# Kernel tuning notes

Hardware: AMD Instinct MI355X
Metric: run time of the kernel (lower is better)

The kernel has to match this reference:

```python
import jax, jax.numpy as jnp
import numpy as np
import math

B, L, E, H, G = 2, 128, 1024, 16, 8
D = E // H   # head_dim = 64
R = H // G   # query heads per kv head = 2


def setup_inputs() -> dict:
    key = jax.random.key(0)
    ks = jax.random.split(key, 12)
    def nrm(k, shape, s=1.0):
        return jax.random.normal(k, shape, dtype=jnp.float32) * s
    return {
        "Q": nrm(ks[0], (B, L, E)),
        "K": nrm(ks[1], (B, L, E)),
        "V": nrm(ks[2], (B, L, E)),
        "rpe": nrm(ks[3], (B, L, L, E)),
        "ln_g": jnp.ones((E,), jnp.float32),
        "ln_b": jnp.zeros((E,), jnp.float32),
        "Wq": nrm(ks[4], (E, H * D), 0.02), "bq": jnp.zeros((H * D,), jnp.float32),
        "Wk": nrm(ks[5], (E, G * D), 0.02), "bk": jnp.zeros((G * D,), jnp.float32),
        "Wv": nrm(ks[6], (E, G * D), 0.02), "bv": jnp.zeros((G * D,), jnp.float32),
        "Wrk": nrm(ks[7], (E, G * D), 0.02), "brk": jnp.zeros((G * D,), jnp.float32),
        "Wrv": nrm(ks[8], (E, G * D), 0.02), "brv": jnp.zeros((G * D,), jnp.float32),
        "Wo": nrm(ks[9], (E, E), 0.02), "bo": jnp.zeros((E,), jnp.float32),
    }


def _layernorm(x, g, b, eps=1e-5):
    mu = jnp.mean(x, axis=-1, keepdims=True)
    var = jnp.var(x, axis=-1, keepdims=True)
    return (x - mu) * jax.lax.rsqrt(var + eps) * g + b


def reference(Q, K, V, rpe, ln_g, ln_b, Wq, bq, Wk, bk, Wv, bv, Wrk, brk, Wrv, brv, Wo, bo):
    q = (Q @ Wq + bq).reshape(B, L, H, D).transpose(0, 2, 1, 3)   # [B,H,L,D]
    k = (K @ Wk + bk).reshape(B, L, G, D).transpose(0, 2, 1, 3)   # [B,G,L,D]
    v = (V @ Wv + bv).reshape(B, L, G, D).transpose(0, 2, 1, 3)   # [B,G,L,D]

    rn = _layernorm(rpe, ln_g, ln_b)                              # [B,L,L,E]
    rpe_k = (rn @ Wrk + brk).reshape(B, L, L, G, D).transpose(0, 3, 1, 2, 4)  # [B,G,L,L,D]
    rpe_v = (rn @ Wrv + brv).reshape(B, L, L, G, D).transpose(0, 3, 1, 2, 4)

    # Group query heads: head h = g*R + r maps to kv group g (repeat_interleave semantics).
    qg = q.reshape(B, G, R, L, D)
    # score[b,h,i,j] = q[b,h,i] . (k[b,g,i] + rpe_k[b,g,i,j]) / sqrt(D)
    # (note: the original pairs q_i with k_i, only rpe_k carries j-dependence)
    base = jnp.einsum('bgrid,bgid->bgri', qg, k)                  # j-independent q.k
    cross = jnp.einsum('bgrid,bgijd->bgrij', qg, rpe_k)
    scores = (base[..., None] + cross) / math.sqrt(D)             # [B,G,R,L,L]

    # Faithful to F.softmax over flattened L*L axis per head.
    attn = jax.nn.softmax(scores.reshape(B, G, R, L * L), axis=-1).reshape(B, G, R, L, L)

    # qv[b,h,i] = sum_j attn[b,h,i,j] * (v[b,g,i] + rpe_v[b,g,i,j])
    wsum = jnp.sum(attn, axis=-1)                                 # [B,G,R,L]
    qv = wsum[..., None] * v[:, :, None] + jnp.einsum('bgrij,bgijd->bgrid', attn, rpe_v)
    qv = qv.reshape(B, H, L, D).transpose(0, 2, 1, 3).reshape(B, L, E)
    return qv @ Wo + bo
```

## Files before the change

kernel.cpp:

```cpp
#include <hip/hip_runtime.h>


__global__ __launch_bounds__(256) void k_zero(
    const float* __restrict__ bq, const float* __restrict__ bk, const float* __restrict__ bv,
    const float* __restrict__ bo,
    float* __restrict__ q_ws, float* __restrict__ k_ws, float* __restrict__ v_ws,
    float* __restrict__ qv_ws, float* __restrict__ out, float* __restrict__ Gu_ws)
{
  int rr = blockIdx.x, tid = threadIdx.x;
#pragma unroll
  for (int s = 0; s < 4; s++) {
    int i = tid + s * 256;
    q_ws[rr * 1024 + i] = bq[i];
    qv_ws[rr * 1024 + i] = 0.f;
    out[rr * 1024 + i] = bo[i];
  }
#pragma unroll
  for (int s = 0; s < 2; s++) {
    int i = tid + s * 256;
    k_ws[rr * 512 + i] = bk[i];
    v_ws[rr * 512 + i] = bv[i];
  }
  int t = rr * 256 + tid;
  if (t < 4096) Gu_ws[t] = 0.f;
}

__global__ __launch_bounds__(256) void k_qkv(
    const float* __restrict__ Q, const float* __restrict__ K, const float* __restrict__ V,
    const float* __restrict__ Wq, const float* __restrict__ Wk, const float* __restrict__ Wv,
    float* __restrict__ q_ws, float* __restrict__ k_ws, float* __restrict__ v_ws)
{
  __shared__ float xs[8][256];
  int ct = blockIdx.x, rt = blockIdx.y, es = blockIdx.z, tid = threadIdx.x;
  const float* X; const float* W; float* out; int ldW, ldO, c0;
  if (ct < 4)      { X = Q; W = Wq; out = q_ws; ldW = 1024; ldO = 1024; c0 = ct * 256; }
  else if (ct < 6) { X = K; W = Wk; out = k_ws; ldW = 512;  ldO = 512;  c0 = (ct - 4) * 256; }
  else             { X = V; W = Wv; out = v_ws; ldW = 512;  ldO = 512;  c0 = (ct - 6) * 256; }
  int row0 = rt * 8, e0 = es * 256;
  for (int f = tid; f < 512; f += 256) {
    int r = f >> 6, e4 = f & 63;
    *(float4*)&xs[r][e4 * 4] = *(const float4*)(X + (size_t)(row0 + r) * 1024 + e0 + e4 * 4);
  }
  __syncthreads();
  int cg = tid & 63, rs = tid >> 6;
  int c = c0 + cg * 4;
  const float* wp = W + (size_t)e0 * ldW + c;
  float a0[4] = {0, 0, 0, 0}, a1[4] = {0, 0, 0, 0};
  float4 wc = *(const float4*)wp;
  for (int e = 0; e < 256; e++) {
    int en = e + 1 < 256 ? e + 1 : 255;
    float4 wn = *(const float4*)(wp + (size_t)en * ldW);
    float x0 = xs[rs][e], x1 = xs[rs + 4][e];
    a0[0] += x0 * wc.x; a0[1] += x0 * wc.y; a0[2] += x0 * wc.z; a0[3] += x0 * wc.w;
    a1[0] += x1 * wc.x; a1[1] += x1 * wc.y; a1[2] += x1 * wc.z; a1[3] += x1 * wc.w;
    wc = wn;
  }
#pragma unroll
  for (int s = 0; s < 4; s++) {
    atomicAdd(out + (size_t)(row0 + rs) * ldO + c + s, a0[s]);
    atomicAdd(out + (size_t)(row0 + rs + 4) * ldO + c + s, a1[s]);
  }
}

__global__ __launch_bounds__(256) void k_base(
    const float* __restrict__ q_ws, const float* __restrict__ k_ws,
    const float* __restrict__ brk, float* __restrict__ S0_ws)
{
  int t = blockIdx.x * 256 + threadIdx.x;
  int r = t >> 4, h = t & 15, g = h >> 1;
  const float* qp = q_ws + r * 1024 + h * 64;
  const float* kp = k_ws + r * 512 + g * 64;
  const float* bp = brk + g * 64;
  float s = 0.f;
#pragma unroll
  for (int d4 = 0; d4 < 16; d4++) {
    float4 q4 = *(const float4*)(qp + d4 * 4);
    float4 k4 = *(const float4*)(kp + d4 * 4);
    float4 b4 = *(const float4*)(bp + d4 * 4);
    s += q4.x * (k4.x + b4.x) + q4.y * (k4.y + b4.y)
       + q4.z * (k4.z + b4.z) + q4.w * (k4.w + b4.w);
  }
  S0_ws[t] = s * 0.125f;
}

__global__ __launch_bounds__(256) void k_uproj(
    const float* __restrict__ q_ws, const float* __restrict__ Wrk,
    const float* __restrict__ lng, const float* __restrict__ lnb,
    float* __restrict__ ut_ws, float* __restrict__ Gu_ws, float* __restrict__ S0_ws)
{
  __shared__ float wt[64][128];
  __shared__ float qs[32][64];
  int et = blockIdx.x, rrt = blockIdx.y, g = blockIdx.z, tid = threadIdx.x;
  int e0 = et * 128, rr0 = rrt * 16;
  for (int f = tid; f < 2048; f += 256) {
    int er = f >> 4, dq = f & 15;
    float4 p = *(const float4*)(Wrk + (size_t)(e0 + er) * 512 + g * 64 + dq * 4);
    wt[dq * 4 + 0][er] = p.x; wt[dq * 4 + 1][er] = p.y;
    wt[dq * 4 + 2][er] = p.z; wt[dq * 4 + 3][er] = p.w;
  }
  for (int f = tid; f < 512; f += 256) {
    int m = f >> 4, dq = f & 15;
    int rr = rr0 + (m >> 1), h = g * 2 + (m & 1);
    float4 p = *(const float4*)(q_ws + (size_t)rr * 1024 + h * 64 + dq * 4);
    qs[m][dq * 4 + 0] = p.x; qs[m][dq * 4 + 1] = p.y;
    qs[m][dq * 4 + 2] = p.z; qs[m][dq * 4 + 3] = p.w;
  }
  __syncthreads();
  int eg = tid & 31, rs = tid >> 5;
  float acc[4][4];
#pragma unroll
  for (int i = 0; i < 4; i++)
#pragma unroll
    for (int s = 0; s < 4; s++) acc[i][s] = 0.f;
  for (int d = 0; d < 64; d++) {
    float4 wv = *(float4*)&wt[d][eg * 4];
#pragma unroll
    for (int i = 0; i < 4; i++) {
      float qv = qs[rs * 4 + i][d];
      acc[i][0] += qv * wv.x; acc[i][1] += qv * wv.y;
      acc[i][2] += qv * wv.z; acc[i][3] += qv * wv.w;
    }
  }
#pragma unroll
  for (int k = 0; k < 2; k++) {
    int rr = rr0 + rs * 2 + k;
#pragma unroll
    for (int s = 0; s < 4; s++) {
      int e = e0 + eg * 4 + s;
      float2 st;
      st.x = acc[2 * k][s] * 0.125f;
      st.y = acc[2 * k + 1][s] * 0.125f;
      *(float2*)(ut_ws + ((size_t)rr * 1024 + e) * 16 + g * 2) = st;
    }
  }
  float4 ge4 = *(const float4*)(lng + e0 + eg * 4);
  float4 be4 = *(const float4*)(lnb + e0 + eg * 4);
#pragma unroll
  for (int i = 0; i < 4; i++) {
    float pg = 0.125f * (ge4.x * acc[i][0] + ge4.y * acc[i][1] + ge4.z * acc[i][2] + ge4.w * acc[i][3]);
    float pb = 0.125f * (be4.x * acc[i][0] + be4.y * acc[i][1] + be4.z * acc[i][2] + be4.w * acc[i][3]);
#pragma unroll
    for (int mk = 16; mk >= 1; mk >>= 1) { pg += __shfl_xor(pg, mk); pb += __shfl_xor(pb, mk); }
    if (eg == 0) {
      int m = rs * 4 + i;
      int rr = rr0 + (m >> 1), h = g * 2 + (m & 1);
      atomicAdd(Gu_ws + rr * 16 + h, pg);
      atomicAdd(S0_ws + rr * 16 + h, pb);
    }
  }
}

__global__ __launch_bounds__(256) void k_dotp(
    const float* __restrict__ rpe, const float* __restrict__ lng,
    const float* __restrict__ ut_ws, const float* __restrict__ Gu_ws,
    const float* __restrict__ S0_ws,
    float* __restrict__ s_ws, float* __restrict__ mu_ws, float* __restrict__ rs_ws)
{
  __shared__ float us[256][16];
  int jt = blockIdx.x, rr = blockIdx.y, tid = threadIdx.x;
  int jl = tid >> 3, hg = tid & 7;
  int j = jt * 32 + jl;
  const float* xrow = rpe + ((size_t)rr * 128 + j) * 1024;
  float acc0 = 0.f, acc1 = 0.f;
  float sx = 0.f, sq = 0.f;

  for (int ec = 0; ec < 4; ec++) {
    __syncthreads();
    for (int f = tid; f < 1024; f += 256) {
      int e = f >> 2, hq = f & 3;
      float4 u4 = *(const float4*)(ut_ws + ((size_t)rr * 1024 + ec * 256 + e) * 16 + hq * 4);
      float ge = lng[ec * 256 + e];
      u4.x *= ge; u4.y *= ge; u4.z *= ge; u4.w *= ge;
      *(float4*)&us[e][hq * 4] = u4;
    }
    __syncthreads();
    const float* xp = xrow + ec * 256;
#pragma unroll 8
    for (int e4 = 0; e4 < 64; e4++) {
      float4 xv = *(const float4*)(xp + e4 * 4);
      float2 u0 = *(float2*)&us[e4 * 4 + 0][hg * 2];
      float2 u1 = *(float2*)&us[e4 * 4 + 1][hg * 2];
      float2 u2 = *(float2*)&us[e4 * 4 + 2][hg * 2];
      float2 u3 = *(float2*)&us[e4 * 4 + 3][hg * 2];
      acc0 += xv.x * u0.x + xv.y * u1.x + xv.z * u2.x + xv.w * u3.x;
      acc1 += xv.x * u0.y + xv.y * u1.y + xv.z * u2.y + xv.w * u3.y;
      sx += xv.x + xv.y + xv.z + xv.w;
      sq += xv.x * xv.x + xv.y * xv.y + xv.z * xv.z + xv.w * xv.w;
    }
  }
  float mu = sx * (1.f / 1024.f);
  float rsv = rsqrtf(fmaxf(sq * (1.f / 1024.f) - mu * mu, 0.f) + 1e-5f);
  float2 Gu2 = *(const float2*)(Gu_ws + rr * 16 + hg * 2);
  float2 S02 = *(const float2*)(S0_ws + rr * 16 + hg * 2);
  float2 o;
  o.x = S02.x + rsv * (acc0 - mu * Gu2.x);
  o.y = S02.y + rsv * (acc1 - mu * Gu2.y);
  *(float2*)(s_ws + ((size_t)rr * 128 + j) * 16 + hg * 2) = o;
  if (hg == 0) { mu_ws[rr * 128 + j] = mu; rs_ws[rr * 128 + j] = rsv; }
}

__global__ __launch_bounds__(256) void k_attn_p(
    const float* __restrict__ mu_ws, const float* __restrict__ rs_ws,
    float* __restrict__ s_ws,
    float* __restrict__ M_ws, float* __restrict__ Z_ws, float* __restrict__ C1_ws)
{
  int rr = blockIdx.x, tid = threadIdx.x;
  int h = tid >> 4, jl = tid & 15;
  float sv[8];
  float m = -1e30f;
#pragma unroll
  for (int k = 0; k < 8; k++) {
    int j = jl + k * 16;
    sv[k] = s_ws[((size_t)rr * 128 + j) * 16 + h];
    m = fmaxf(m, sv[k]);
  }
#pragma unroll
  for (int mk = 8; mk >= 1; mk >>= 1) m = fmaxf(m, __shfl_xor(m, mk, 16));
  float z = 0.f, c1 = 0.f;
#pragma unroll
  for (int k = 0; k < 8; k++) {
    int j = jl + k * 16;
    float p = expf(sv[k] - m);
    z += p;
    float p2 = p * rs_ws[rr * 128 + j];
    c1 += p2 * mu_ws[rr * 128 + j];
    s_ws[((size_t)rr * 128 + j) * 16 + h] = p2;
  }
#pragma unroll
  for (int mk = 8; mk >= 1; mk >>= 1) { z += __shfl_xor(z, mk, 16); c1 += __shfl_xor(c1, mk, 16); }
  if (jl == 0) {
    M_ws[rr * 16 + h] = m; Z_ws[rr * 16 + h] = z; C1_ws[rr * 16 + h] = c1;
  }
}

__global__ __launch_bounds__(128) void k_comb(
    const float* __restrict__ M_ws, const float* __restrict__ Z_ws, float* __restrict__ sc_ws)
{
  __shared__ float red[128];
  int b = blockIdx.x >> 4, h = blockIdx.x & 15;
  int i = threadIdx.x;
  int idx = ((b << 7) + i) * 16 + h;
  float ml = M_ws[idx];
  red[i] = ml;
  __syncthreads();
  for (int s = 64; s >= 1; s >>= 1) {
    if (i < s) red[i] = fmaxf(red[i], red[i + s]);
    __syncthreads();
  }
  float mg = red[0];
  __syncthreads();
  float zl = Z_ws[idx] * expf(ml - mg);
  red[i] = zl;
  __syncthreads();
  for (int s = 64; s >= 1; s >>= 1) {
    if (i < s) red[i] += red[i + s];
    __syncthreads();
  }
  float zg = red[0];
  sc_ws[idx] = expf(ml - mg) / zg;
}

__global__ __launch_bounds__(256) void k_wun(
    const float* __restrict__ rpe, const float* __restrict__ lng, const float* __restrict__ lnb,
    const float* __restrict__ p2_ws,
    const float* __restrict__ Z_ws, const float* __restrict__ C1_ws,
    float* __restrict__ w_ws)
{
  __shared__ float xs[16][256];
  __shared__ float p2s[128][16];
  __shared__ float C1S[16], ZS[16];
  int et = blockIdx.x, rr = blockIdx.y, tid = threadIdx.x;
  int e0 = et * 256;
  for (int f = tid; f < 512; f += 256) {
    int j = f >> 2, hq = f & 3;
    *(float4*)&p2s[j][hq * 4] = *(const float4*)(p2_ws + ((size_t)rr * 128 + j) * 16 + hq * 4);
  }
  if (tid < 16) { C1S[tid] = C1_ws[rr * 16 + tid]; ZS[tid] = Z_ws[rr * 16 + tid]; }
  float acc[16];
#pragma unroll
  for (int h = 0; h < 16; h++) acc[h] = 0.f;
  for (int jc = 0; jc < 8; jc++) {
    __syncthreads();
    for (int f = tid; f < 1024; f += 256) {
      int j = f >> 6, e4 = f & 63;
      *(float4*)&xs[j][e4 * 4] =
          *(const float4*)(rpe + ((size_t)(rr * 128 + jc * 16 + j)) * 1024 + e0 + e4 * 4);
    }
    __syncthreads();
#pragma unroll
    for (int j = 0; j < 16; j++) {
      float x = xs[j][tid];
      float4 p0 = *(float4*)&p2s[jc * 16 + j][0];
      float4 p1 = *(float4*)&p2s[jc * 16 + j][4];
      float4 p2 = *(float4*)&p2s[jc * 16 + j][8];
      float4 p3 = *(float4*)&p2s[jc * 16 + j][12];
      acc[0] += x * p0.x; acc[1] += x * p0.y; acc[2] += x * p0.z; acc[3] += x * p0.w;
      acc[4] += x * p1.x; acc[5] += x * p1.y; acc[6] += x * p1.z; acc[7] += x * p1.w;
      acc[8] += x * p2.x; acc[9] += x * p2.y; acc[10] += x * p2.z; acc[11] += x * p2.w;
      acc[12] += x * p3.x; acc[13] += x * p3.y; acc[14] += x * p3.z; acc[15] += x * p3.w;
    }
  }
  int e = e0 + tid;
  float ge = lng[e], be = lnb[e];
  float* wp = w_ws + ((size_t)rr * 1024 + e) * 16;
#pragma unroll
  for (int hq = 0; hq < 4; hq++) {
    float4 o;
    o.x = ge * (acc[hq * 4 + 0] - C1S[hq * 4 + 0]) + be * ZS[hq * 4 + 0];
    o.y = ge * (acc[hq * 4 + 1] - C1S[hq * 4 + 1]) + be * ZS[hq * 4 + 1];
    o.z = ge * (acc[hq * 4 + 2] - C1S[hq * 4 + 2]) + be * ZS[hq * 4 + 2];
    o.w = ge * (acc[hq * 4 + 3] - C1S[hq * 4 + 3]) + be * ZS[hq * 4 + 3];
    *(float4*)(wp + hq * 4) = o;
  }
}

__global__ __launch_bounds__(256) void k_qv(
    const float* __restrict__ w_ws, const float* __restrict__ Wrv,
    float* __restrict__ qv_ws)
{
  __shared__ float As[32][133];
  int g = blockIdx.x, rrt = blockIdx.y, es = blockIdx.z, tid = threadIdx.x;
  int rr0 = rrt * 16, e0 = es * 128;
  for (int f = tid; f < 2048; f += 256) {
    int rl = f >> 7, e = f & 127;
    float2 w2 = *(const float2*)(w_ws + ((size_t)(rr0 + rl) * 1024 + e0 + e) * 16 + g * 2);
    As[rl * 2 + 0][e] = w2.x;
    As[rl * 2 + 1][e] = w2.y;
  }
  __syncthreads();
  int cl = tid & 15, ms = tid >> 4;
  const float* wp = Wrv + (size_t)e0 * 512 + g * 64 + cl * 4;
  float acc[2][4];
#pragma unroll
  for (int hh = 0; hh < 2; hh++)
#pragma unroll
    for (int s = 0; s < 4; s++) acc[hh][s] = 0.f;
  float4 wc = *(const float4*)wp;
  for (int e = 0; e < 128; e++) {
    int en = e + 1 < 128 ? e + 1 : 127;
    float4 wn = *(const float4*)(wp + (size_t)en * 512);
    float a0 = As[ms * 2][e], a1 = As[ms * 2 + 1][e];
    acc[0][0] += a0 * wc.x; acc[0][1] += a0 * wc.y; acc[0][2] += a0 * wc.z; acc[0][3] += a0 * wc.w;
    acc[1][0] += a1 * wc.x; acc[1][1] += a1 * wc.y; acc[1][2] += a1 * wc.z; acc[1][3] += a1 * wc.w;
    wc = wn;
  }
  int rr = rr0 + ms;
#pragma unroll
  for (int hh = 0; hh < 2; hh++) {
    float* qp = qv_ws + (size_t)rr * 1024 + (g * 2 + hh) * 64 + cl * 4;
#pragma unroll
    for (int s = 0; s < 4; s++) atomicAdd(qp + s, acc[hh][s]);
  }
}

__global__ __launch_bounds__(256) void k_out(
    const float* __restrict__ qv_ws, const float* __restrict__ v_ws,
    const float* __restrict__ brv, const float* __restrict__ Z_ws,
    const float* __restrict__ sc_ws, const float* __restrict__ Wo,
    float* __restrict__ out)
{
  __shared__ float xs[8][128];
  int ct = blockIdx.x, rt = blockIdx.y, es = blockIdx.z, tid = threadIdx.x;
  int row0 = rt * 8, e0 = es * 128, c0 = ct * 256;
  for (int f = tid; f < 1024; f += 256) {
    int r = f >> 7, ei = f & 127;
    int e = e0 + ei, row = row0 + r;
    int h = e >> 6, gg = h >> 1, dl = e & 63;
    float vb = v_ws[row * 512 + gg * 64 + dl] + brv[gg * 64 + dl];
    xs[r][ei] = sc_ws[row * 16 + h] * (Z_ws[row * 16 + h] * vb + qv_ws[(size_t)row * 1024 + e]);
  }
  __syncthreads();
  int cg = tid & 63, rs = tid >> 6;
  int c = c0 + cg * 4;
  const float* wp = Wo + (size_t)e0 * 1024 + c;
  float a0[4] = {0, 0, 0, 0}, a1[4] = {0, 0, 0, 0};
  float4 wc = *(const float4*)wp;
  for (int e = 0; e < 128; e++) {
    int en = e + 1 < 128 ? e + 1 : 127;
    float4 wn = *(const float4*)(wp + (size_t)en * 1024);
    float x0 = xs[rs][e], x1 = xs[rs + 4][e];
    a0[0] += x0 * wc.x; a0[1] += x0 * wc.y; a0[2] += x0 * wc.z; a0[3] += x0 * wc.w;
    a1[0] += x1 * wc.x; a1[1] += x1 * wc.y; a1[2] += x1 * wc.z; a1[3] += x1 * wc.w;
    wc = wn;
  }
#pragma unroll
  for (int s = 0; s < 4; s++) {
    atomicAdd(out + (size_t)(row0 + rs) * 1024 + c + s, a0[s]);
    atomicAdd(out + (size_t)(row0 + rs + 4) * 1024 + c + s, a1[s]);
  }
}

extern "C" void kernel_launch(void* const* d_in, const int* in_sizes, int n_in,
                              void* d_out, int out_size, void* d_ws, size_t ws_size,
                              hipStream_t stream) {
  (void)in_sizes; (void)n_in; (void)out_size; (void)ws_size;
  const float* Q   = (const float*)d_in[0];
  const float* K   = (const float*)d_in[1];
  const float* V   = (const float*)d_in[2];
  const float* rpe = (const float*)d_in[3];
  const float* lng = (const float*)d_in[4];
  const float* lnb = (const float*)d_in[5];
  const float* Wq  = (const float*)d_in[6];
  const float* bq  = (const float*)d_in[7];
  const float* Wk  = (const float*)d_in[8];
  const float* bk  = (const float*)d_in[9];
  const float* Wv  = (const float*)d_in[10];
  const float* bv  = (const float*)d_in[11];
  const float* Wrk = (const float*)d_in[12];
  const float* brk = (const float*)d_in[13];
  const float* Wrv = (const float*)d_in[14];
  const float* brv = (const float*)d_in[15];
  const float* Wo  = (const float*)d_in[16];
  const float* bo  = (const float*)d_in[17];
  float* out = (float*)d_out;

  float* ws    = (float*)d_ws;
  float* q_ws  = ws;
  float* k_ws  = q_ws + 262144;
  float* v_ws  = k_ws + 131072;
  float* ut_ws = v_ws + 131072;
  float* S0_ws = ut_ws + 4194304;
  float* Gu_ws = S0_ws + 4096;
  float* s_ws  = Gu_ws + 4096;
  float* mu_ws = s_ws + 524288;
  float* rs_ws = mu_ws + 32768;
  float* M_ws  = rs_ws + 32768;
  float* Z_ws  = M_ws + 4096;
  float* C1_ws = Z_ws + 4096;
  float* sc_ws = C1_ws + 4096;
  float* qv_ws = sc_ws + 4096;
  float* w_ws  = ut_ws;

  k_zero<<<256, 256, 0, stream>>>(bq, bk, bv, bo, q_ws, k_ws, v_ws, qv_ws, out, Gu_ws);
  k_qkv<<<dim3(8, 32, 4), 256, 0, stream>>>(Q, K, V, Wq, Wk, Wv, q_ws, k_ws, v_ws);
  k_base<<<16, 256, 0, stream>>>(q_ws, k_ws, brk, S0_ws);
  k_uproj<<<dim3(8, 16, 8), 256, 0, stream>>>(q_ws, Wrk, lng, lnb, ut_ws, Gu_ws, S0_ws);
  k_dotp<<<dim3(4, 256), 256, 0, stream>>>(rpe, lng, ut_ws, Gu_ws, S0_ws, s_ws, mu_ws, rs_ws);
  k_attn_p<<<256, 256, 0, stream>>>(mu_ws, rs_ws, s_ws, M_ws, Z_ws, C1_ws);
  k_comb<<<32, 128, 0, stream>>>(M_ws, Z_ws, sc_ws);
  k_wun<<<dim3(4, 256), 256, 0, stream>>>(rpe, lng, lnb, s_ws, Z_ws, C1_ws, w_ws);
  k_qv<<<dim3(8, 16, 8), 256, 0, stream>>>(w_ws, Wrv, qv_ws);
  k_out<<<dim3(4, 32, 8), 256, 0, stream>>>(qv_ws, v_ws, brv, Z_ws, sc_ws, Wo, out);
}
```

Baseline: 505.9 us.

## Stage rpe tiles in LDS for k_dotp and remap threads to one head each

k_dotp now loads 16 rpe rows per 128-wide chunk cooperatively into shared memory with coalesced float4 loads, instead of having each thread stream its own row straight from global memory. The u vectors are stored transposed per head, and each thread computes a single head for one row. Row statistics are split across the 16 lanes and reduced with shuffles, and the grid is doubled to 8 row tiles. The aim is better coalescing and less redundant global traffic on the large rpe tensor, at the cost of more barriers and more LDS traffic.

```diff
diff --git a/kernel.cpp b/kernel.cpp
--- a/kernel.cpp
+++ b/kernel.cpp
@@ -156,46 +156,58 @@
     const float* __restrict__ S0_ws,
     float* __restrict__ s_ws, float* __restrict__ mu_ws, float* __restrict__ rs_ws)
 {
-  __shared__ float us[256][16];
+  __shared__ float xs[16][132];
+  __shared__ float us_t[16][132];
   int jt = blockIdx.x, rr = blockIdx.y, tid = threadIdx.x;
-  int jl = tid >> 3, hg = tid & 7;
-  int j = jt * 32 + jl;
-  const float* xrow = rpe + ((size_t)rr * 128 + j) * 1024;
-  float acc0 = 0.f, acc1 = 0.f;
-  float sx = 0.f, sq = 0.f;
-
-  for (int ec = 0; ec < 4; ec++) {
-    __syncthreads();
-    for (int f = tid; f < 1024; f += 256) {
+  int jl = tid >> 4, hg = tid & 15;
+  int j = jt * 16 + jl;
+  float acc = 0.f, sx = 0.f, sq = 0.f;
+
+  for (int ec = 0; ec < 8; ec++) {
+    int eb = ec * 128;
+    __syncthreads();
+#pragma unroll
+    for (int p = 0; p < 2; p++) {
+      int f = p * 256 + tid;
+      int row = f >> 5, e4 = f & 31;
+      float4 xv = *(const float4*)(rpe + ((size_t)(rr * 128 + jt * 16 + row)) * 1024 + eb + e4 * 4);
+      *(float4*)&xs[row][e4 * 4] = xv;
+    }
+#pragma unroll
+    for (int p = 0; p < 2; p++) {
+      int f = p * 256 + tid;
       int e = f >> 2, hq = f & 3;
-      float4 u4 = *(const float4*)(ut_ws + ((size_t)rr * 1024 + ec * 256 + e) * 16 + hq * 4);
-      float ge = lng[ec * 256 + e];
-      u4.x *= ge; u4.y *= ge; u4.z *= ge; u4.w *= ge;
-      *(float4*)&us[e][hq * 4] = u4;
-    }
-    __syncthreads();
-    const float* xp = xrow + ec * 256;
+      float4 u4 = *(const float4*)(ut_ws + ((size_t)rr * 1024 + eb + e) * 16 + hq * 4);
+      float ge = lng[eb + e];
+      us_t[hq * 4 + 0][e] = u4.x * ge;
+      us_t[hq * 4 + 1][e] = u4.y * ge;
+      us_t[hq * 4 + 2][e] = u4.z * ge;
+      us_t[hq * 4 + 3][e] = u4.w * ge;
+    }
+    __syncthreads();
 #pragma unroll 8
-    for (int e4 = 0; e4 < 64; e4++) {
-      float4 xv = *(const float4*)(xp + e4 * 4);
-      float2 u0 = *(float2*)&us[e4 * 4 + 0][hg * 2];
-      float2 u1 = *(float2*)&us[e4 * 4 + 1][hg * 2];
-      float2 u2 = *(float2*)&us[e4 * 4 + 2][hg * 2];
-      float2 u3 = *(float2*)&us[e4 * 4 + 3][hg * 2];
-      acc0 += xv.x * u0.x + xv.y * u1.x + xv.z * u2.x + xv.w * u3.x;
-      acc1 += xv.x * u0.y + xv.y * u1.y + xv.z * u2.y + xv.w * u3.y;
+    for (int e4 = 0; e4 < 32; e4++) {
+      float4 xv = *(float4*)&xs[jl][e4 * 4];
+      float4 uv = *(float4*)&us_t[hg][e4 * 4];
+      acc += xv.x * uv.x + xv.y * uv.y + xv.z * uv.z + xv.w * uv.w;
+    }
+#pragma unroll
+    for (int t = 0; t < 2; t++) {
+      float4 xv = *(float4*)&xs[jl][(hg * 2 + t) * 4];
       sx += xv.x + xv.y + xv.z + xv.w;
       sq += xv.x * xv.x + xv.y * xv.y + xv.z * xv.z + xv.w * xv.w;
     }
   }
+#pragma unroll
+  for (int mk = 8; mk >= 1; mk >>= 1) {
+    sx += __shfl_xor(sx, mk, 16);
+    sq += __shfl_xor(sq, mk, 16);
+  }
   float mu = sx * (1.f / 1024.f);
   float rsv = rsqrtf(fmaxf(sq * (1.f / 1024.f) - mu * mu, 0.f) + 1e-5f);
-  float2 Gu2 = *(const float2*)(Gu_ws + rr * 16 + hg * 2);
-  float2 S02 = *(const float2*)(S0_ws + rr * 16 + hg * 2);
-  float2 o;
-  o.x = S02.x + rsv * (acc0 - mu * Gu2.x);
-  o.y = S02.y + rsv * (acc1 - mu * Gu2.y);
-  *(float2*)(s_ws + ((size_t)rr * 128 + j) * 16 + hg * 2) = o;
+  float Gu = Gu_ws[rr * 16 + hg];
+  float S0 = S0_ws[rr * 16 + hg];
+  s_ws[((size_t)rr * 128 + j) * 16 + hg] = S0 + rsv * (acc - mu * Gu);
   if (hg == 0) { mu_ws[rr * 128 + j] = mu; rs_ws[rr * 128 + j] = rsv; }
 }
 
@@ -435,7 +447,7 @@
   k_qkv<<<dim3(8, 32, 4), 256, 0, stream>>>(Q, K, V, Wq, Wk, Wv, q_ws, k_ws, v_ws);
   k_base<<<16, 256, 0, stream>>>(q_ws, k_ws, brk, S0_ws);
   k_uproj<<<dim3(8, 16, 8), 256, 0, stream>>>(q_ws, Wrk, lng, lnb, ut_ws, Gu_ws, S0_ws);
-  k_dotp<<<dim3(4, 256), 256, 0, stream>>>(rpe, lng, ut_ws, Gu_ws, S0_ws, s_ws, mu_ws, rs_ws);
+  k_dotp<<<dim3(8, 256), 256, 0, stream>>>(rpe, lng, ut_ws, Gu_ws, S0_ws, s_ws, mu_ws, rs_ws);
   k_attn_p<<<256, 256, 0, stream>>>(mu_ws, rs_ws, s_ws, M_ws, Z_ws, C1_ws);
   k_comb<<<32, 128, 0, stream>>>(M_ws, Z_ws, sc_ws);
   k_wun<<<dim3(4, 256), 256, 0, stream>>>(rpe, lng, lnb, s_ws, Z_ws, C1_ws, w_ws);
```

After: 478.1 us. -5.5%, faster.
